# Optimization experiments

Measured on AMD Instinct MI355X. Metric: run time of the kernel, lower is better.

## Reference

```python
import jax, jax.numpy as jnp
import numpy as np

N, E, D, F, L = 50000, 250000, 128, 12, 4
EPS_POS = 1e-6
EPS_LN = 1e-5


def setup_inputs() -> dict:
    key = jax.random.key(0)
    ks = iter(jax.random.split(key, 40))
    w = lambda *s: jax.random.normal(next(ks), s, dtype=jnp.float32) * 0.05
    inp = {
        'node_features': jax.random.normal(next(ks), (N, F), dtype=jnp.float32),
        'pos': jax.random.normal(next(ks), (N, 2), dtype=jnp.float32),
        'edge_attr_raw': jax.random.normal(next(ks), (E, F), dtype=jnp.float32),
        'node_proj_w': w(F, D), 'node_proj_b': jnp.zeros((D,), jnp.float32),
        'edge_proj_w': w(F, D), 'edge_proj_b': jnp.zeros((D,), jnp.float32),
        'edge_w1': w(L, 2 * D + 1, D), 'edge_b1': jnp.zeros((L, D), jnp.float32),
        'edge_w2': w(L, D, D), 'edge_b2': jnp.zeros((L, D), jnp.float32),
        'node_w1': w(L, 2 * D, D), 'node_b1': jnp.zeros((L, D), jnp.float32),
        'node_w2': w(L, D, D), 'node_b2': jnp.zeros((L, D), jnp.float32),
        'pos_w1': w(L, D + 1, 1), 'pos_b1': jnp.zeros((L, 1), jnp.float32),
        'pos_w2': w(L, 1, 1), 'pos_b2': jnp.zeros((L, 1), jnp.float32),
        'ln_g': jnp.ones((D,), jnp.float32), 'ln_b': jnp.zeros((D,), jnp.float32),
        'edge_index': jax.random.randint(next(ks), (2, E), 0, N, dtype=jnp.int32),
    }
    return inp


def reference(node_features, pos, edge_attr_raw,
              node_proj_w, node_proj_b, edge_proj_w, edge_proj_b,
              edge_w1, edge_b1, edge_w2, edge_b2,
              node_w1, node_b1, node_w2, node_b2,
              pos_w1, pos_b1, pos_w2, pos_b2,
              ln_g, ln_b, edge_index):
    src, tgt = edge_index[0], edge_index[1]
    n = node_features.shape[0]
    x = node_features @ node_proj_w + node_proj_b          # [N, D]
    # edge_projection output is concatenated then sliced away in the original
    # (edge_input[:, :2D+1]); it is mathematically dead but computed faithfully.
    _edge_attr = edge_attr_raw @ edge_proj_w + edge_proj_b  # dead
    p = pos                                                  # [N, 2]
    for l in range(L):
        xs, xt = x[src], x[tgt]                              # [E, D]
        ps, pt = p[src], p[tgt]                              # [E, 2]
        dist = jnp.linalg.norm(ps - pt, axis=1, keepdims=True)  # [E, 1]
        e_in = jnp.concatenate([xs, xt, dist], axis=1)       # [E, 2D+1]
        msg = jax.nn.silu(e_in @ edge_w1[l] + edge_b1[l]) @ edge_w2[l] + edge_b2[l]
        pos_diff = pt - ps
        pos_unit = pos_diff / (jnp.linalg.norm(pos_diff, axis=1, keepdims=True) + EPS_POS)
        pw = jax.nn.silu(jnp.concatenate([msg, dist], axis=1) @ pos_w1[l] + pos_b1[l])
        pw = pw @ pos_w2[l] + pos_b2[l]                       # [E, 1]
        p = p + jax.ops.segment_sum(pos_unit * pw, tgt, num_segments=n)
        agg = jax.ops.segment_sum(msg, tgt, num_segments=n)  # [N, D]
        n_in = jnp.concatenate([x, agg], axis=1)              # [N, 2D]
        x = x + (jax.nn.silu(n_in @ node_w1[l] + node_b1[l]) @ node_w2[l] + node_b2[l])
    mu = jnp.mean(x, axis=-1, keepdims=True)
    var = jnp.mean(jnp.square(x - mu), axis=-1, keepdims=True)
    x = (x - mu) * jax.lax.rsqrt(var + EPS_LN) * ln_g + ln_b
    return x[None]                                            # [1, N, D]
```

## Files before the change

### kernel.cpp

```cpp
#include <hip/hip_runtime.h>
#include <hip/hip_bf16.h>


#define NNODES 50000
#define NEDGES 250000
#define NTILES 3125
#define SGRID  768
#define MGRID  256

typedef unsigned short u16;
typedef __attribute__((ext_vector_type(8))) short bf16x8;
typedef __attribute__((ext_vector_type(4))) float floatx4;

__device__ __forceinline__ float b2f(u16 h){ unsigned u=((unsigned)h)<<16; float f; __builtin_memcpy(&f,&u,4); return f; }
__device__ __forceinline__ u16 f2b(float f){ unsigned u; __builtin_memcpy(&u,&f,4); u = u + 0x7FFFu + ((u>>16)&1u); return (u16)(u>>16); }
__device__ __forceinline__ float siluf(float x){ return x*__builtin_amdgcn_rcpf(1.f+__expf(-x)); }
__device__ __forceinline__ float ldf(const void* p, long i, int isbf){
  return isbf ? b2f(((const u16*)p)[i]) : ((const float*)p)[i];
}
__device__ __forceinline__ long swz(long row, int col){
  return (row>>4)*2048 + (long)(((col>>4)*4 + (int)(row&3))*64 + (((int)(row&15))>>2)*16 + (col&15));
}

__global__ void detect_kernel(const void* lng, int* flag){
  if (threadIdx.x==0 && blockIdx.x==0) *flag = (((const u16*)lng)[0] != 0) ? 1 : 0;
}

#define SU_W12   192
#define SU_EBW   704
#define SU_W2P   708
#define SU_PPARM 712
#define SU_PROJ  713
#define SU_CVTP  25713
#define SU_END   26104
__global__ __launch_bounds__(256) void setup_kernel(
    const void* __restrict__ ew1, const void* __restrict__ ew2,
    const void* __restrict__ nw1, const void* __restrict__ nw2,
    u16* __restrict__ packed,
    const void* __restrict__ eb2, const void* __restrict__ pw1,
    const void* __restrict__ pb1, const void* __restrict__ pw2v, const void* __restrict__ pb2,
    float* __restrict__ w2p, float* __restrict__ c2p, float* __restrict__ pparm,
    float* __restrict__ ebW,
    const void* __restrict__ nf, const void* __restrict__ npw, const void* __restrict__ npb,
    u16* __restrict__ xb,
    const void* __restrict__ pos, float* __restrict__ pf,
    const int* __restrict__ flagp)
{
  const int isbf = *flagp;
  const int b = blockIdx.x, tid = threadIdx.x;
  __shared__ float red[128];
  if (b < SU_W12){
    int t = b*256 + tid;
    int m = t >> 11; int r = t & 2047;
    int lane = r & 63; int ntk = r >> 6;
    int kk = ntk >> 3, nt = ntk & 7;
    int l = m/6, w = m%6;
    const void* src; long off;
    switch(w){
      case 0: src=ew1; off=(long)l*257*128;            break;
      case 1: src=ew1; off=(long)l*257*128 + 128*128;  break;
      case 2: src=ew2; off=(long)l*128*128;            break;
      case 3: src=nw1; off=(long)l*256*128;            break;
      case 4: src=nw1; off=(long)l*256*128 + 128*128;  break;
      default:src=nw2; off=(long)l*128*128;            break;
    }
    int c  = nt*16 + (lane & 15);
    int k0 = kk*32 + (lane >> 4)*8;
    u16 vals[8];
#pragma unroll
    for (int j=0;j<8;j++){
      long idx = off + (long)(k0+j)*128 + c;
      vals[j] = isbf ? ((const u16*)src)[idx] : f2b(((const float*)src)[idx]);
    }
    bf16x8 v; __builtin_memcpy(&v, vals, 16);
    *(bf16x8*)(packed + (long)t*8) = v;
  } else if (b < SU_EBW){
    int bb = b - SU_W12;
    int l = bb >> 7, k = bb & 127;
    if (tid < 128){
      int j = tid;
      long e2 = (long)l*16384 + (long)k*128;
      long nb = (long)l*256*128 + 128*128;
      float acc = 0.f;
      for (int d=0; d<128; d++)
        acc += ldf(ew2, e2 + d, isbf) * ldf(nw1, nb + (long)d*128 + j, isbf);
      int kk = k>>5, lane = ((k>>3)&3)*16 + (j&15), nt = j>>4, jj = k&7;
      packed[(long)(24+l)*16384 + (long)((kk*8+nt)*64 + lane)*8 + jj] = f2b(acc);
    }
  } else if (b < SU_W2P){
    int l = b - SU_EBW;
    if (tid < 128){
      int j = tid;
      long nb = (long)l*256*128 + 128*128;
      float acc = 0.f;
      for (int d=0; d<128; d++)
        acc += ldf(eb2, (long)l*128 + d, isbf) * ldf(nw1, nb + (long)d*128 + j, isbf);
      ebW[l*128+j] = acc;
    }
  } else if (b < SU_PPARM){
    int l = b - SU_W2P;
    int i = tid;
    long Woff = (long)l*128*128, poff = (long)l*129;
    if (i < 128){
      float acc = 0.f;
      for (int j=0;j<128;j++) acc += ldf(ew2, Woff + (long)i*128 + j, isbf) * ldf(pw1, poff + j, isbf);
      w2p[l*128+i] = acc;
      red[i] = ldf(eb2, (long)l*128 + i, isbf) * ldf(pw1, poff + i, isbf);
    }
    __syncthreads();
    for (int st=64; st>0; st>>=1){ if (i<st) red[i]+=red[i+st]; __syncthreads(); }
    if (i==0) c2p[l] = red[0];
  } else if (b == SU_PPARM){
    int l = tid;
    if (l < 4){
      pparm[l*4+0] = ldf(pw1, (long)l*129 + 128, isbf);
      pparm[l*4+1] = ldf(pb1, l, isbf);
      pparm[l*4+2] = ldf(pw2v, l, isbf);
      pparm[l*4+3] = ldf(pb2, l, isbf);
    }
  } else if (b < SU_CVTP){
    int n = (b - SU_PROJ)*2 + (tid>>7), d = tid & 127;
    if (n < NNODES){
      float acc = ldf(npb, d, isbf);
#pragma unroll
      for (int f=0; f<12; f++) acc += ldf(nf, (long)n*12+f, isbf) * ldf(npw, f*128+d, isbf);
      xb[swz(n, d)] = f2b(acc);
    }
  } else {
    int i = (b - SU_CVTP)*256 + tid;
    if (i < 2*NNODES) pf[i] = ldf(pos, i, isbf);
  }
}

__global__ __launch_bounds__(256) void hist_kernel(const int* __restrict__ tgt, int* __restrict__ cnt, int E){
  int i = blockIdx.x*256 + threadIdx.x;
  if (i < E) atomicAdd(&cnt[tgt[i]], 1);
}

__global__ __launch_bounds__(256) void bsum_kernel(const int* __restrict__ cnt, int* __restrict__ bsum, int N){
  int i = blockIdx.x*256 + threadIdx.x;
  int v = (i < N) ? cnt[i] : 0;
#pragma unroll
  for (int off=32; off; off>>=1) v += __shfl_down(v, off);
  __shared__ int ws[4];
  if ((threadIdx.x & 63) == 0) ws[threadIdx.x>>6] = v;
  __syncthreads();
  if (threadIdx.x == 0) bsum[blockIdx.x] = ws[0]+ws[1]+ws[2]+ws[3];
}

__global__ __launch_bounds__(256) void bscan_kernel(int* __restrict__ bsum, int nb){
  __shared__ int lds[256];
  int i = threadIdx.x;
  int v = (i < nb) ? bsum[i] : 0;
  lds[i] = v; __syncthreads();
#pragma unroll
  for (int off=1; off<256; off<<=1){
    int t = (i>=off)? lds[i-off] : 0; __syncthreads();
    lds[i] += t; __syncthreads();
  }
  if (i < nb) bsum[i] = lds[i] - v;
}

__global__ __launch_bounds__(256) void csr_kernel(
    const int* __restrict__ cnt, const int* __restrict__ bsum,
    int* __restrict__ rowptr, int* __restrict__ cursor, float* __restrict__ degf, int N)
{
  __shared__ int lds[256];
  int i = blockIdx.x*256 + threadIdx.x;
  int c = (i < N) ? cnt[i] : 0;
  lds[threadIdx.x] = c; __syncthreads();
#pragma unroll
  for (int off=1; off<256; off<<=1){
    int t = (threadIdx.x>=off)? lds[threadIdx.x-off] : 0; __syncthreads();
    lds[threadIdx.x] += t; __syncthreads();
  }
  int run = bsum[blockIdx.x] + lds[threadIdx.x] - c;
  if (i < N){
    rowptr[i] = run; cursor[i] = run; degf[i] = (float)c;
    if (i == N-1) rowptr[N] = run + c;
  }
}

__global__ __launch_bounds__(256) void scatter_kernel(
    const int* __restrict__ src, const int* __restrict__ tgt,
    int* __restrict__ cursor, int* __restrict__ permsrc, int E)
{
  int e = blockIdx.x*256 + threadIdx.x;
  if (e >= E) return;
  int t = tgt[e];
  int p = atomicAdd(&cursor[t], 1);
  permsrc[p] = src[e];
}

__global__ __launch_bounds__(256, 3) void mm_single_kernel(
    const u16* __restrict__ X, const u16* __restrict__ W,
    const void* __restrict__ bias, long bias_off, int hasbias,
    u16* __restrict__ Out, const int* __restrict__ flagp)
{
  extern __shared__ u16 dls[];
  u16* wl = dls;
  const int tid = threadIdx.x, wave = tid>>6, lane = tid&63;
  const int isbf = *flagp;
  const int lr = lane&15, lg = lane>>4;
  u16* sw = dls + 16384 + (wave<<11);
  for (int i=tid; i<2048; i+=256)
    *(bf16x8*)(wl + (long)i*8) = *(const bf16x8*)(W + (long)i*8);
  float biasv[8];
#pragma unroll
  for (int nt=0;nt<8;nt++) biasv[nt] = hasbias ? ldf(bias, bias_off + nt*16 + lr, isbf) : 0.f;
  int aoff[4];
#pragma unroll
  for (int kk=0;kk<4;kk++) aoff[kk] = ((2*kk + (lg>>1))*4 + (lr&3))*64 + (lr>>2)*16 + (lg&1)*8;
  __syncthreads();
  for (int tile = blockIdx.x*4 + wave; tile < NTILES; tile += SGRID*4){
    const u16* xt = X + (long)tile*2048;
    bf16x8 a[4];
#pragma unroll
    for (int kk=0;kk<4;kk++) a[kk] = *(const bf16x8*)(xt + aoff[kk]);
    floatx4 acc[8];
#pragma unroll
    for (int i=0;i<8;i++) acc[i]=(floatx4){0,0,0,0};
#pragma unroll
    for (int kk=0;kk<4;kk++){
#pragma unroll
      for (int nt=0;nt<8;nt++){
        bf16x8 b = *(const bf16x8*)(wl + ((kk*8+nt)*64 + lane)*8);
        acc[nt] = __builtin_amdgcn_mfma_f32_16x16x32_bf16(a[kk], b, acc[nt], 0, 0, 0);
      }
    }
    u16* ot = Out + (long)tile*2048;
#pragma unroll
    for (int r=0;r<4;r++){
#pragma unroll
      for (int nt=0;nt<8;nt++) sw[(lg*4+r)*128 + nt*16 + lr] = f2b(acc[nt][r] + biasv[nt]);
    }
#pragma unroll
    for (int j=0;j<4;j++){
      bf16x8 v = *(const bf16x8*)(sw + j*512 + lane*8);
      *(bf16x8*)(ot + j*512 + lane*8) = v;
    }
  }
}

template<int LN>
__global__ __launch_bounds__(512, 2) void mega_kernel(
    const u16* X, const u16* __restrict__ H,
    const u16* __restrict__ W1, const u16* __restrict__ W12, const u16* __restrict__ W2,
    const void* __restrict__ nb1, long nb1_off,
    const void* __restrict__ nb2, long nb2_off,
    const float* __restrict__ degf, const float* __restrict__ ebW,
    u16* xb,
    const void* __restrict__ lng, const void* __restrict__ lnb, void* __restrict__ outp,
    const int* __restrict__ flagp)
{
  extern __shared__ u16 dls[];
  u16* w1s  = dls;
  u16* w12s = dls + 16384;
  u16* w2s  = dls + 32768;
  const int tid = threadIdx.x, wave = tid>>6, lane = tid&63;
  const int isbf = *flagp;
  const int lr = lane&15, lg = lane>>4;
  u16* stg = dls + 49152 + wave*2176;
  for (int i=tid; i<2048; i+=512){
    *(bf16x8*)(w1s  + (long)i*8) = *(const bf16x8*)(W1  + (long)i*8);
    *(bf16x8*)(w12s + (long)i*8) = *(const bf16x8*)(W12 + (long)i*8);
    *(bf16x8*)(w2s  + (long)i*8) = *(const bf16x8*)(W2  + (long)i*8);
  }
  float nb1v[8], nb2v[8], ebv[8];
#pragma unroll
  for (int nt=0;nt<8;nt++){
    int col = nt*16 + lr;
    nb1v[nt] = ldf(nb1, nb1_off + col, isbf);
    nb2v[nt] = ldf(nb2, nb2_off + col, isbf);
    ebv[nt]  = ebW[col];
  }
  float gv[8], bvv[8];
  if (LN){
#pragma unroll
    for (int nt=0;nt<8;nt++){ int col=nt*16+lr; gv[nt]=ldf(lng,col,isbf); bvv[nt]=ldf(lnb,col,isbf); }
  }
  int aoff[4];
#pragma unroll
  for (int kk=0;kk<4;kk++) aoff[kk] = ((2*kk + (lg>>1))*4 + (lr&3))*64 + (lr>>2)*16 + (lg&1)*8;
  __syncthreads();
  for (int tile = blockIdx.x*8 + wave; tile < NTILES; tile += MGRID*8){
    const u16* xt = X + (long)tile*2048;
    const u16* hr = H + ((long)tile*16 + lr)*128;
    bf16x8 ax[4], ah[4];
#pragma unroll
    for (int kk=0;kk<4;kk++){
      ax[kk] = *(const bf16x8*)(xt + aoff[kk]);
      ah[kk] = *(const bf16x8*)(hr + kk*32 + lg*8);
    }
    floatx4 acc[8];
#pragma unroll
    for (int i=0;i<8;i++) acc[i]=(floatx4){0,0,0,0};
#pragma unroll
    for (int kk=0;kk<4;kk++){
#pragma unroll
      for (int nt=0;nt<8;nt++){
        bf16x8 b1 = *(const bf16x8*)(w1s + ((kk*8+nt)*64 + lane)*8);
        acc[nt] = __builtin_amdgcn_mfma_f32_16x16x32_bf16(ax[kk], b1, acc[nt], 0, 0, 0);
        bf16x8 b2 = *(const bf16x8*)(w12s + ((kk*8+nt)*64 + lane)*8);
        acc[nt] = __builtin_amdgcn_mfma_f32_16x16x32_bf16(ah[kk], b2, acc[nt], 0, 0, 0);
      }
    }
    float dv[4];
#pragma unroll
    for (int r=0;r<4;r++) dv[r] = degf[(long)tile*16 + lg*4 + r];
#pragma unroll
    for (int r=0;r<4;r++){
#pragma unroll
      for (int nt=0;nt<8;nt++)
        stg[(lg*4+r)*136 + nt*16 + lr] = f2b(siluf(acc[nt][r] + nb1v[nt] + dv[r]*ebv[nt]));
    }
    bf16x8 ha[4];
#pragma unroll
    for (int kk=0;kk<4;kk++) ha[kk] = *(const bf16x8*)(stg + lr*136 + kk*32 + lg*8);
    floatx4 acc2[8];
#pragma unroll
    for (int i=0;i<8;i++) acc2[i]=(floatx4){0,0,0,0};
#pragma unroll
    for (int kk=0;kk<4;kk++){
#pragma unroll
      for (int nt=0;nt<8;nt++){
        bf16x8 b = *(const bf16x8*)(w2s + ((kk*8+nt)*64 + lane)*8);
        acc2[nt] = __builtin_amdgcn_mfma_f32_16x16x32_bf16(ha[kk], b, acc2[nt], 0, 0, 0);
      }
    }
    u16* xo = xb + (long)tile*2048;
#pragma unroll
    for (int r=0;r<4;r++){
#pragma unroll
      for (int nt=0;nt<8;nt++){
        int o = (nt*4+r)*64 + lane;
        float v = acc2[nt][r] + nb2v[nt] + b2f(xo[o]);
        acc2[nt][r] = v;
        if (!LN) xo[o] = f2b(v);
      }
    }
    if (LN){
      float s[4] = {0,0,0,0}, q[4] = {0,0,0,0};
#pragma unroll
      for (int r=0;r<4;r++){
#pragma unroll
        for (int nt=0;nt<8;nt++){ float v = acc2[nt][r]; s[r] += v; q[r] += v*v; }
      }
#pragma unroll
      for (int mask=1; mask<16; mask<<=1){
#pragma unroll
        for (int r=0;r<4;r++){ s[r] += __shfl_xor(s[r], mask); q[r] += __shfl_xor(q[r], mask); }
      }
      float mu4[4], inv4[4];
#pragma unroll
      for (int r=0;r<4;r++){
        float mu = s[r]*(1.f/128.f);
        float var = q[r]*(1.f/128.f) - mu*mu;
        mu4[r] = mu; inv4[r] = rsqrtf(var + 1e-5f);
      }
      if (isbf){
#pragma unroll
        for (int r=0;r<4;r++){
#pragma unroll
          for (int nt=0;nt<8;nt++)
            stg[(lg*4+r)*128 + nt*16 + lr] = f2b((acc2[nt][r]-mu4[r])*inv4[r]*gv[nt] + bvv[nt]);
        }
        u16* ot = (u16*)outp + (long)tile*2048;
#pragma unroll
        for (int j=0;j<4;j++){
          bf16x8 v = *(const bf16x8*)(stg + j*512 + lane*8);
          *(bf16x8*)(ot + j*512 + lane*8) = v;
        }
      } else {
#pragma unroll
        for (int r=0;r<4;r++){
          long row = (long)tile*16 + lg*4 + r;
#pragma unroll
          for (int nt=0;nt<8;nt++){
            int col = nt*16 + lr;
            ((float*)outp)[row*128+col] = (acc2[nt][r]-mu4[r])*inv4[r]*gv[nt] + bvv[nt];
          }
        }
      }
    }
  }
}

__global__ __launch_bounds__(256) void agg_kernel(
    const int* __restrict__ rowptr, const int* __restrict__ permsrc,
    const float* __restrict__ pf_in,
    const u16* __restrict__ A, const u16* __restrict__ B,
    const void* __restrict__ ew1, long w1c_off,
    const float* __restrict__ w2p, const float* __restrict__ c2pl,
    const float* __restrict__ pp,
    u16* __restrict__ Hb, float* __restrict__ pf_out, int N,
    const int* __restrict__ flagp)
{
  const int isbf = *flagp;
  int tid = threadIdx.x, lane = tid & 63;
  int t = blockIdx.x*4 + (tid>>6);
  if (t >= N) return;
  int tu = __builtin_amdgcn_readfirstlane(t);
  float c0 = ldf(ew1, w1c_off + 2*lane,     isbf);
  float c1 = ldf(ew1, w1c_off + 2*lane + 1, isbf);
  float2 wp = *(const float2*)(w2p + 2*lane);
  float c2 = c2pl[0];
  float p0 = pp[0], p1 = pp[1], p2 = pp[2], p3 = pp[3];
  int jb = rowptr[tu], je = rowptr[tu+1];
  float2 pt = *(const float2*)(pf_in + 2*(long)tu);
  unsigned bv = *(const unsigned*)(B + (long)tu*128 + 2*lane);
  float b0 = b2f((u16)bv), b1 = b2f((u16)(bv>>16));
  float h0a = 0.f, h1a = 0.f, dpx = 0.f, dpy = 0.f;
  for (int j0 = jb; j0 < je; j0 += 4){
    int m = je - j0; if (m > 4) m = 4;
    int s[4]; float2 ps[4]; unsigned av[4];
    float part[4], dist[4], dxv[4], dyv[4];
#pragma unroll
    for (int c=0;c<4;c++) if (c<m) s[c] = permsrc[j0+c];
#pragma unroll
    for (int c=0;c<4;c++) if (c<m){
      ps[c] = *(const float2*)(pf_in + 2*(long)s[c]);
      av[c] = *(const unsigned*)(A + (long)s[c]*128 + 2*lane);
    }
#pragma unroll
    for (int c=0;c<4;c++){
      if (c<m){
        float dx = pt.x - ps[c].x, dy = pt.y - ps[c].y;
        float d2 = dx*dx + dy*dy;
        float dd = __builtin_amdgcn_sqrtf(d2);
        float h0 = siluf(b2f((u16)av[c])       + b0 + dd*c0);
        float h1 = siluf(b2f((u16)(av[c]>>16)) + b1 + dd*c1);
        h0a += h0; h1a += h1;
        part[c] = h0*wp.x + h1*wp.y;
        dist[c] = dd; dxv[c] = dx; dyv[c] = dy;
      } else part[c] = 0.f;
    }
#pragma unroll
    for (int off=32; off; off>>=1){
#pragma unroll
      for (int c=0;c<4;c++) part[c] += __shfl_xor(part[c], off);
    }
#pragma unroll
    for (int c=0;c<4;c++){
      if (c<m){
        float spre = part[c] + c2 + dist[c]*p0 + p1;
        float pwv  = siluf(spre)*p2 + p3;
        float inv  = __builtin_amdgcn_rcpf(dist[c] + 1e-6f);
        dpx += dxv[c]*inv*pwv; dpy += dyv[c]*inv*pwv;
      }
    }
  }
  *(unsigned*)(Hb + (long)tu*128 + 2*lane) = (unsigned)f2b(h0a) | ((unsigned)f2b(h1a)<<16);
  if (lane == 0){
    float2 o; o.x = pt.x + dpx; o.y = pt.y + dpy;
    *(float2*)(pf_out + 2*(long)tu) = o;
  }
}

extern "C" void kernel_launch(void* const* d_in, const int* in_sizes, int n_in,
                              void* d_out, int out_size, void* d_ws, size_t ws_size,
                              hipStream_t stream)
{
  const void* nf  = d_in[0];
  const void* pos = d_in[1];
  const void* npw = d_in[3];
  const void* npb = d_in[4];
  const void* ew1 = d_in[7];
  const void* eb1 = d_in[8];
  const void* ew2 = d_in[9];
  const void* eb2 = d_in[10];
  const void* nw1 = d_in[11];
  const void* nb1 = d_in[12];
  const void* nw2 = d_in[13];
  const void* nb2 = d_in[14];
  const void* pw1 = d_in[15];
  const void* pb1 = d_in[16];
  const void* pw2 = d_in[17];
  const void* pb2 = d_in[18];
  const void* lng = d_in[19];
  const void* lnb = d_in[20];
  const int* eidx = (const int*)d_in[21];
  const int N = NNODES, E = NEDGES;
  const int* srcp = eidx;
  const int* tgtp = eidx + E;

  char* w = (char*)d_ws;
  size_t off = 0;
  auto alloc = [&](size_t bytes)->char* { char* p = w + off; off += (bytes + 255)/256*256; return p; };
  u16*   xb    = (u16*)  alloc((size_t)N*128*2);
  u16*   Ab    = (u16*)  alloc((size_t)N*128*2);
  u16*   Bb    = (u16*)  alloc((size_t)N*128*2);
  u16*   Hb    = (u16*)  alloc((size_t)N*128*2);
  float* pf0   = (float*)alloc((size_t)N*2*4);
  float* pf1   = (float*)alloc((size_t)N*2*4);
  int*   cnt   = (int*)  alloc((size_t)N*4);
  int*   rowptr= (int*)  alloc((size_t)(N+1)*4);
  int*   cursor= (int*)  alloc((size_t)N*4);
  float* degf  = (float*)alloc((size_t)N*4);
  int*   perm  = (int*)  alloc((size_t)E*4);
  int*   bsum  = (int*)  alloc(256*4);
  u16*   pk    = (u16*)  alloc((size_t)28*16384*2);
  float* ebW   = (float*)alloc(4*128*4);
  float* w2p   = (float*)alloc(4*128*4);
  float* c2p   = (float*)alloc(4*4);
  float* pparm = (float*)alloc(16*4);
  int*   flag  = (int*)  alloc(4);

  const int NB = (N + 255)/256;
  detect_kernel<<<1, 64, 0, stream>>>(lng, flag);
  hipMemsetAsync(cnt, 0, (size_t)N*4, stream);
  hist_kernel<<<(E+255)/256, 256, 0, stream>>>(tgtp, cnt, E);
  bsum_kernel<<<NB, 256, 0, stream>>>(cnt, bsum, N);
  bscan_kernel<<<1, 256, 0, stream>>>(bsum, NB);
  csr_kernel<<<NB, 256, 0, stream>>>(cnt, bsum, rowptr, cursor, degf, N);
  scatter_kernel<<<(E+255)/256, 256, 0, stream>>>(srcp, tgtp, cursor, perm, E);
  setup_kernel<<<SU_END, 256, 0, stream>>>(
      ew1, ew2, nw1, nw2, pk,
      eb2, pw1, pb1, pw2, pb2,
      w2p, c2p, pparm, ebW,
      nf, npw, npb, xb,
      pos, pf0, flag);

  mm_single_kernel<<<SGRID, 256, 49152, stream>>>(xb, pk + 0*16384, eb1, 0, 1, Ab, flag);
  mm_single_kernel<<<SGRID, 256, 49152, stream>>>(xb, pk + 1*16384, nullptr, 0, 0, Bb, flag);
  for (int l = 0; l < 4; l++){
    const u16* NW1a = pk + (l*6+3)*16384;
    const u16* NW2p = pk + (l*6+5)*16384;
    const u16* W12p = pk + (24+l)*16384;
    float* pin  = (l & 1) ? pf1 : pf0;
    float* pout = (l & 1) ? pf0 : pf1;

    agg_kernel<<<(N+3)/4, 256, 0, stream>>>(
        rowptr, perm, pin, Ab, Bb,
        ew1, (long)l*257*128 + 256*128,
        w2p + l*128, c2p + l, pparm + l*4,
        Hb, pout, N, flag);
    if (l < 3){
      mega_kernel<0><<<MGRID, 512, 133120, stream>>>(
          xb, Hb, NW1a, W12p, NW2p, nb1, (long)l*128, nb2, (long)l*128,
          degf, ebW + l*128, xb, nullptr, nullptr, nullptr, flag);
      mm_single_kernel<<<SGRID, 256, 49152, stream>>>(
          xb, pk + ((l+1)*6+0)*16384, eb1, (long)(l+1)*128, 1, Ab, flag);
      mm_single_kernel<<<SGRID, 256, 49152, stream>>>(
          xb, pk + ((l+1)*6+1)*16384, nullptr, 0, 0, Bb, flag);
    } else {
      mega_kernel<1><<<MGRID, 512, 133120, stream>>>(
          xb, Hb, NW1a, W12p, NW2p, nb1, (long)l*128, nb2, (long)l*128,
          degf, ebW + l*128, xb, lng, lnb, d_out, flag);
    }
  }
}
```

Measured before the change: 459.5 us.

## Make agg kernel grid-stride persistent and spread per-edge scalar work across lanes

The aggregation kernel now launches a fixed grid of 2048 blocks, and each wave loops over target nodes with a grid stride. Before, one block was launched per four nodes. Per-edge position loads, distance, and the position-weight math now run on four lanes in parallel instead of redundantly on all 64. The distances are broadcast with readlane, and the dp partials are reduced with shuffles at the end. This is meant to cut launch and block-setup overhead and redundant scalar work, at the cost of extra selects and shuffles.

```diff
diff --git a/kernel.cpp b/kernel.cpp
--- a/kernel.cpp
+++ b/kernel.cpp
@@ -7,6 +7,8 @@
 #define NTILES 3125
 #define SGRID  768
 #define MGRID  256
+#define AGGRID 2048
+#define AGWAVES (AGGRID*4)
 
 typedef unsigned short u16;
 typedef __attribute__((ext_vector_type(8))) short bf16x8;
@@ -17,6 +19,12 @@
 __device__ __forceinline__ float siluf(float x){ return x*__builtin_amdgcn_rcpf(1.f+__expf(-x)); }
 __device__ __forceinline__ float ldf(const void* p, long i, int isbf){
   return isbf ? b2f(((const u16*)p)[i]) : ((const float*)p)[i];
+}
+__device__ __forceinline__ float rdlane(float v, int l){
+  int i; __builtin_memcpy(&i,&v,4);
+  int r = __builtin_amdgcn_readlane(i, l);
+  float f; __builtin_memcpy(&f,&r,4);
+  return f;
 }
 __device__ __forceinline__ long swz(long row, int col){
   return (row>>4)*2048 + (long)(((col>>4)*4 + (int)(row&3))*64 + (((int)(row&15))>>2)*16 + (col&15));
@@ -398,62 +406,63 @@
 {
   const int isbf = *flagp;
   int tid = threadIdx.x, lane = tid & 63;
-  int t = blockIdx.x*4 + (tid>>6);
-  if (t >= N) return;
-  int tu = __builtin_amdgcn_readfirstlane(t);
+  int wid = blockIdx.x*4 + (tid>>6);
+  const int cc = lane & 3;
   float c0 = ldf(ew1, w1c_off + 2*lane,     isbf);
   float c1 = ldf(ew1, w1c_off + 2*lane + 1, isbf);
   float2 wp = *(const float2*)(w2p + 2*lane);
   float c2 = c2pl[0];
   float p0 = pp[0], p1 = pp[1], p2 = pp[2], p3 = pp[3];
-  int jb = rowptr[tu], je = rowptr[tu+1];
-  float2 pt = *(const float2*)(pf_in + 2*(long)tu);
-  unsigned bv = *(const unsigned*)(B + (long)tu*128 + 2*lane);
-  float b0 = b2f((u16)bv), b1 = b2f((u16)(bv>>16));
-  float h0a = 0.f, h1a = 0.f, dpx = 0.f, dpy = 0.f;
-  for (int j0 = jb; j0 < je; j0 += 4){
-    int m = je - j0; if (m > 4) m = 4;
-    int s[4]; float2 ps[4]; unsigned av[4];
-    float part[4], dist[4], dxv[4], dyv[4];
-#pragma unroll
-    for (int c=0;c<4;c++) if (c<m) s[c] = permsrc[j0+c];
-#pragma unroll
-    for (int c=0;c<4;c++) if (c<m){
-      ps[c] = *(const float2*)(pf_in + 2*(long)s[c]);
-      av[c] = *(const unsigned*)(A + (long)s[c]*128 + 2*lane);
-    }
-#pragma unroll
-    for (int c=0;c<4;c++){
-      if (c<m){
-        float dx = pt.x - ps[c].x, dy = pt.y - ps[c].y;
-        float d2 = dx*dx + dy*dy;
-        float dd = __builtin_amdgcn_sqrtf(d2);
-        float h0 = siluf(b2f((u16)av[c])       + b0 + dd*c0);
-        float h1 = siluf(b2f((u16)(av[c]>>16)) + b1 + dd*c1);
-        h0a += h0; h1a += h1;
-        part[c] = h0*wp.x + h1*wp.y;
-        dist[c] = dd; dxv[c] = dx; dyv[c] = dy;
-      } else part[c] = 0.f;
-    }
-#pragma unroll
-    for (int off=32; off; off>>=1){
-#pragma unroll
-      for (int c=0;c<4;c++) part[c] += __shfl_xor(part[c], off);
-    }
-#pragma unroll
-    for (int c=0;c<4;c++){
-      if (c<m){
-        float spre = part[c] + c2 + dist[c]*p0 + p1;
-        float pwv  = siluf(spre)*p2 + p3;
-        float inv  = __builtin_amdgcn_rcpf(dist[c] + 1e-6f);
-        dpx += dxv[c]*inv*pwv; dpy += dyv[c]*inv*pwv;
-      }
-    }
-  }
-  *(unsigned*)(Hb + (long)tu*128 + 2*lane) = (unsigned)f2b(h0a) | ((unsigned)f2b(h1a)<<16);
-  if (lane == 0){
-    float2 o; o.x = pt.x + dpx; o.y = pt.y + dpy;
-    *(float2*)(pf_out + 2*(long)tu) = o;
+  for (int t = wid; t < N; t += AGWAVES){
+    int tu = __builtin_amdgcn_readfirstlane(t);
+    int jb = rowptr[tu], je = rowptr[tu+1];
+    float2 pt = *(const float2*)(pf_in + 2*(long)tu);
+    unsigned bv = *(const unsigned*)(B + (long)tu*128 + 2*lane);
+    float b0 = b2f((u16)bv), b1 = b2f((u16)(bv>>16));
+    float h0a = 0.f, h1a = 0.f, dpx = 0.f, dpy = 0.f;
+    for (int j0 = jb; j0 < je; j0 += 4){
+      int m = je - j0; if (m > 4) m = 4;
+      int s[4];
+#pragma unroll
+      for (int c=0;c<4;c++) s[c] = permsrc[j0 + (c<m ? c : 0)];
+      int scc = cc==0 ? s[0] : (cc==1 ? s[1] : (cc==2 ? s[2] : s[3]));
+      float2 psc = *(const float2*)(pf_in + 2*(long)scc);
+      float dxc = pt.x - psc.x, dyc = pt.y - psc.y;
+      float ddc = __builtin_amdgcn_sqrtf(dxc*dxc + dyc*dyc);
+      float dd_s[4];
+#pragma unroll
+      for (int c=0;c<4;c++) dd_s[c] = rdlane(ddc, c);
+      unsigned av[4];
+#pragma unroll
+      for (int c=0;c<4;c++) if (c<m) av[c] = *(const unsigned*)(A + (long)s[c]*128 + 2*lane);
+      float part[4];
+#pragma unroll
+      for (int c=0;c<4;c++){
+        if (c<m){
+          float h0 = siluf(b2f((u16)av[c])       + b0 + dd_s[c]*c0);
+          float h1 = siluf(b2f((u16)(av[c]>>16)) + b1 + dd_s[c]*c1);
+          h0a += h0; h1a += h1;
+          part[c] = h0*wp.x + h1*wp.y;
+        } else part[c] = 0.f;
+      }
+#pragma unroll
+      for (int off=32; off; off>>=1){
+#pragma unroll
+        for (int c=0;c<4;c++) part[c] += __shfl_xor(part[c], off);
+      }
+      float pc = cc==0 ? part[0] : (cc==1 ? part[1] : (cc==2 ? part[2] : part[3]));
+      float sprec = pc + c2 + ddc*p0 + p1;
+      float pwvc  = siluf(sprec)*p2 + p3;
+      float invc  = __builtin_amdgcn_rcpf(ddc + 1e-6f);
+      if (cc < m){ dpx += dxc*invc*pwvc; dpy += dyc*invc*pwvc; }
+    }
+    *(unsigned*)(Hb + (long)tu*128 + 2*lane) = (unsigned)f2b(h0a) | ((unsigned)f2b(h1a)<<16);
+    dpx += __shfl_xor(dpx, 1); dpx += __shfl_xor(dpx, 2);
+    dpy += __shfl_xor(dpy, 1); dpy += __shfl_xor(dpy, 2);
+    if (lane == 0){
+      float2 o; o.x = pt.x + dpx; o.y = pt.y + dpy;
+      *(float2*)(pf_out + 2*(long)tu) = o;
+    }
   }
 }
 
@@ -530,7 +539,7 @@
     float* pin  = (l & 1) ? pf1 : pf0;
     float* pout = (l & 1) ? pf0 : pf1;
 
-    agg_kernel<<<(N+3)/4, 256, 0, stream>>>(
+    agg_kernel<<<AGGRID, 256, 0, stream>>>(
         rowptr, perm, pin, Ab, Bb,
         ew1, (long)l*257*128 + 256*128,
         w2p + l*128, c2p + l, pparm + l*4,
```

Result: faster. 446.6 us (-2.8%).
